# Performance work log

Measured on AMD Instinct MI355X. Metric: run time of the kernel, lower is better.

Reference implementation:

```python
import jax, jax.numpy as jnp
import numpy as np

HEADS = 8
HIDDEN = 1536
HEAD_DIM = HIDDEN // HEADS
SCALE = HEAD_DIM ** -0.5


def setup_inputs() -> dict:
    key = jax.random.key(0)
    ks = jax.random.split(key, 10)
    B, S_IMG, S_TXT = 32, 1024, 77
    w = 0.02
    return {
        "img": jax.random.normal(ks[0], (B, S_IMG, HIDDEN), dtype=jnp.float32),
        "text": jax.random.normal(ks[1], (B, S_TXT, HIDDEN), dtype=jnp.float32),
        "Wq": jax.random.normal(ks[2], (HIDDEN, HIDDEN), dtype=jnp.float32) * w,
        "bq": jnp.zeros((HIDDEN,), dtype=jnp.float32),
        "Wk": jax.random.normal(ks[3], (HIDDEN, HIDDEN), dtype=jnp.float32) * w,
        "bk": jnp.zeros((HIDDEN,), dtype=jnp.float32),
        "Wv": jax.random.normal(ks[4], (HIDDEN, HIDDEN), dtype=jnp.float32) * w,
        "bv": jnp.zeros((HIDDEN,), dtype=jnp.float32),
        "Wo": jax.random.normal(ks[5], (HIDDEN, HIDDEN), dtype=jnp.float32) * w,
        "bo": jnp.zeros((HIDDEN,), dtype=jnp.float32),
    }


def reference(img, text, Wq, bq, Wk, bk, Wv, bv, Wo, bo):
    B, Sq, D = img.shape
    Sk = text.shape[1]
    # QKV projections (nn.Linear: y = x @ W.T + b)
    q = img @ Wq.T + bq    # [B, Sq, D]
    k = text @ Wk.T + bk   # [B, Sk, D]
    v = text @ Wv.T + bv
    # detach trick: position 0 of k/v has gradient stopped; forward value unchanged
    k0 = jax.lax.stop_gradient(k[:, :1, :])
    k = jnp.concatenate([k0, k[:, 1:, :]], axis=1)
    v0 = jax.lax.stop_gradient(v[:, :1, :])
    v = jnp.concatenate([v0, v[:, 1:, :]], axis=1)
    # split heads
    q = q.reshape(B, Sq, HEADS, HEAD_DIM)
    k = k.reshape(B, Sk, HEADS, HEAD_DIM)
    v = v.reshape(B, Sk, HEADS, HEAD_DIM)
    # attention scores and probs (mask is None in this module)
    scores = jnp.einsum("bqhd,bkhd->bhqk", q, k) * SCALE  # [B, H, Sq, Sk]
    probs = jax.nn.softmax(scores, axis=-1)
    out = jnp.einsum("bhqk,bkhd->bqhd", probs, v).reshape(B, Sq, D)
    return out @ Wo.T + bo
```

## Files before the change

### kernel.cpp

```cpp
#include <hip/hip_runtime.h>
#include <hip/hip_bf16.h>


typedef unsigned short u16;
typedef _Float16 f16x8 __attribute__((ext_vector_type(8)));
typedef __attribute__((ext_vector_type(8))) short s16x8;
typedef __attribute__((ext_vector_type(4))) float f32x4;
typedef __attribute__((ext_vector_type(4))) short s16x4;

#define MFMAH(a, b, c) __builtin_amdgcn_mfma_f32_16x16x32_f16(a, b, c, 0, 0, 0)

__device__ __forceinline__ u16 f2h(float x) {
    _Float16 h = (_Float16)x;
    return __builtin_bit_cast(u16, h);
}

__device__ __forceinline__ void gload16(const u16* g, const u16* l) {
    __builtin_amdgcn_global_load_lds(
        (const __attribute__((address_space(1))) unsigned int*)g,
        (__attribute__((address_space(3))) unsigned int*)l, 16, 0, 0);
}

__device__ __forceinline__ unsigned ldsa(const u16* p) {
    return (unsigned)(size_t)(const __attribute__((address_space(3))) u16*)p;
}

__device__ __forceinline__ f16x8 dsr128(unsigned byte_addr) {
    f16x8 d;
    asm volatile("ds_read_b128 %0, %1" : "=v"(d) : "v"(byte_addr));
    return d;
}

__device__ __forceinline__ int rh(int r) { return (r >> 1) & 3; }

__global__ void conv_h(const float* __restrict__ x, u16* __restrict__ h, int n8) {
    const int i = blockIdx.x * 256 + threadIdx.x;
    if (i >= n8) return;
    const f32x4 a = ((const f32x4*)x)[2 * i];
    const f32x4 b = ((const f32x4*)x)[2 * i + 1];
    u16 o[8];
#pragma unroll
    for (int j = 0; j < 4; ++j) { o[j] = f2h(a[j]); o[4 + j] = f2h(b[j]); }
    *(s16x8*)&h[(size_t)i << 3] = *(s16x8*)o;
}

struct Conv5Args {
    const float* x[5];
    u16* h[5];
    int n8[5];
};

__global__ void conv_h5(Conv5Args A) {
    const int z = blockIdx.y;
    const int i = blockIdx.x * 256 + threadIdx.x;
    if (i >= A.n8[z]) return;
    const float* x = A.x[z];
    const f32x4 a = ((const f32x4*)x)[2 * i];
    const f32x4 b = ((const f32x4*)x)[2 * i + 1];
    u16 o[8];
#pragma unroll
    for (int j = 0; j < 4; ++j) { o[j] = f2h(a[j]); o[4 + j] = f2h(b[j]); }
    *(s16x8*)&A.h[z][(size_t)i << 3] = *(s16x8*)o;
}

template <int OUTF32>
__global__ __launch_bounds__(512, 2) void gemm_h_nt(
    const u16* __restrict__ A,
    const u16* __restrict__ B0, const float* __restrict__ bias0, void* __restrict__ C0,
    const u16* __restrict__ B1, const float* __restrict__ bias1, void* __restrict__ C1,
    int M, int N, int K, int nby) {
    __shared__ u16 lds[65536];

    const u16* B = B0; const float* bias = bias0; void* Cout = C0;
    if (blockIdx.z) { B = B1; bias = bias1; Cout = C1; }

    const int nwg = gridDim.x;
    const int q8 = nwg >> 3, r8 = nwg & 7;
    const int xcd = blockIdx.x & 7, loc = blockIdx.x >> 3;
    const int wgid = (xcd < r8 ? xcd * (q8 + 1) : r8 * (q8 + 1) + (xcd - r8) * q8) + loc;
    const int bx = wgid / nby, by = wgid - bx * nby;
    const int row0 = bx * 256, col0 = by * 256;

    const int t = threadIdx.x, lane = t & 63, w = t >> 6;
    const int wr = w >> 2, wc = w & 3;
    const int l15 = lane & 15, lhi = lane >> 4;

    const u16* gpA[2]; const u16* gpB[2];
    int lofA[2], lofB[2];
#pragma unroll
    for (int it = 0; it < 2; ++it) {
        const int ci = it * 512 + t;
        const int row = ci >> 2, slot = ci & 3;
        const int gs = slot ^ rh(row);
        int ar = row0 + row; if (ar > M - 1) ar = M - 1;
        gpA[it] = A + (size_t)ar * K + (gs << 3);
        gpB[it] = B + (size_t)(col0 + row) * K + (gs << 3);
        lofA[it] = ci * 8;
        lofB[it] = 8192 + ci * 8;
    }

    const int ss = rh(l15);
    const unsigned lb0 = ldsa(lds);
    unsigned aof[8], bof[4];
#pragma unroll
    for (int i = 0; i < 8; ++i) {
        const int ar = wr * 128 + i * 16 + l15;
        aof[i] = (unsigned)((ar * 32 + ((lhi ^ ss) << 3)) * 2);
    }
#pragma unroll
    for (int n = 0; n < 4; ++n) {
        const int br = wc * 64 + n * 16 + l15;
        bof[n] = (unsigned)((8192 + br * 32 + ((lhi ^ ss) << 3)) * 2);
    }

    f32x4 acc[8][4] = {};
    const int NT = K >> 5;

#define SBAR0() __builtin_amdgcn_sched_barrier(0)
#define BARX()  do { SBAR0(); __builtin_amdgcn_s_barrier(); SBAR0(); } while (0)
#define LGKM0() do { asm volatile("s_waitcnt lgkmcnt(0)" ::: "memory"); SBAR0(); } while (0)

#pragma unroll
    for (int p = 0; p < 3; ++p) {
        const size_t kp = (size_t)p << 5;
        u16* lb = lds + (p << 14);
        gload16(gpA[0] + kp, lb + lofA[0]); gload16(gpA[1] + kp, lb + lofA[1]);
        gload16(gpB[0] + kp, lb + lofB[0]); gload16(gpB[1] + kp, lb + lofB[1]);
    }
    asm volatile("s_waitcnt vmcnt(8)" ::: "memory");
    BARX();

    for (int tt = 0; tt < NT; ++tt) {
        const unsigned cb = lb0 + ((unsigned)(tt & 3) << 15);
        u16* lsb = lds + (((tt + 3) & 3) << 14);
        const int tx = (tt + 3 < NT) ? tt + 3 : tt + 3 - NT;
        const size_t kn = (size_t)tx << 5;

        f16x8 a0[4], a1[4], bb[4];

#pragma unroll
        for (int nf = 0; nf < 4; ++nf) bb[nf] = dsr128(cb + bof[nf]);
#pragma unroll
        for (int mf = 0; mf < 4; ++mf) a0[mf] = dsr128(cb + aof[mf]);
        SBAR0();
        gload16(gpA[0] + kn, lsb + lofA[0]);
        gload16(gpA[1] + kn, lsb + lofA[1]);
        BARX();
        LGKM0();
        __builtin_amdgcn_s_setprio(1);
#pragma unroll
        for (int nf = 0; nf < 4; ++nf)
#pragma unroll
            for (int mf = 0; mf < 4; ++mf)
                acc[mf][nf] = MFMAH(a0[mf], bb[nf], acc[mf][nf]);
        __builtin_amdgcn_s_setprio(0);
        BARX();

#pragma unroll
        for (int mf = 0; mf < 4; ++mf) a1[mf] = dsr128(cb + aof[4 + mf]);
        SBAR0();
        gload16(gpB[0] + kn, lsb + lofB[0]);
        gload16(gpB[1] + kn, lsb + lofB[1]);
        BARX();
        LGKM0();
        __builtin_amdgcn_s_setprio(1);
#pragma unroll
        for (int nf = 0; nf < 4; ++nf)
#pragma unroll
            for (int mf = 0; mf < 4; ++mf)
                acc[4 + mf][nf] = MFMAH(a1[mf], bb[nf], acc[4 + mf][nf]);
        __builtin_amdgcn_s_setprio(0);
        asm volatile("s_waitcnt vmcnt(8)" ::: "memory");
        BARX();
    }
    asm volatile("s_waitcnt vmcnt(0)" ::: "memory");

#pragma unroll
    for (int nf = 0; nf < 4; ++nf) {
        const int col = col0 + wc * 64 + nf * 16 + l15;
        const float bs = bias[col];
#pragma unroll
        for (int mf = 0; mf < 8; ++mf) {
            const int row = row0 + wr * 128 + mf * 16 + (lhi << 2);
#pragma unroll
            for (int r = 0; r < 4; ++r) {
                if (row + r < M) {
                    const float v = acc[mf][nf][r] + bs;
                    if (OUTF32) ((float*)Cout)[(size_t)(row + r) * N + col] = v;
                    else        ((u16*)Cout)[(size_t)(row + r) * N + col] = f2h(v);
                }
            }
        }
    }
#undef SBAR0
#undef BARX
#undef LGKM0
}

#define ALDK 200
#define ALDP 104

__global__ void attn_fused(const u16* __restrict__ qbuf, const u16* __restrict__ kbuf,
                           const u16* __restrict__ vbuf, u16* __restrict__ obuf) {
    __shared__ u16 Ks[80 * ALDK];
    __shared__ u16 Pls[64 * ALDP];
    __shared__ u16 Vt[96 * ALDP];

    const int t = threadIdx.x, lane = t & 63, w = t >> 6;
    const int qt = blockIdx.x, h = blockIdx.y, b = blockIdx.z;
    const int l15 = lane & 15, lhi = lane >> 4;

    f16x8 qf[6];
    {
        const size_t qrow = (size_t)(b * 1024 + qt * 64 + w * 16 + l15);
        const u16* qp = qbuf + qrow * 1536 + h * 192 + (lhi << 3);
#pragma unroll
        for (int kt = 0; kt < 6; ++kt) qf[kt] = *(const f16x8*)(qp + kt * 32);
    }

    for (int c = t; c < 80 * 24; c += 256) {
        const int s = c / 24, d8 = (c - s * 24) << 3;
        s16x8 val = {};
        if (s < 77) val = *(const s16x8*)&kbuf[(size_t)(b * 77 + s) * 1536 + h * 192 + d8];
        *(s16x8*)&Ks[s * ALDK + d8] = val;
    }
    for (int c = t; c < 96 * 12; c += 256) {
        const int s = c % 96, d8 = (c / 96) << 3;
        s16x8 val = {};
        if (s < 77) val = *(const s16x8*)&vbuf[(size_t)(b * 77 + s) * 1536 + h * 192 + d8];
#pragma unroll
        for (int j = 0; j < 8; ++j) Vt[(d8 + j) * ALDP + s] = (u16)val[j];
    }
    {
        const int row = w * 16 + l15;
        s16x4 z = {0, 0, 0, 0};
        *(s16x4*)&Pls[row * ALDP + 80 + (lhi << 2)] = z;
    }
    __syncthreads();

    f32x4 sacc[5] = {};
#pragma unroll
    for (int kt = 0; kt < 6; ++kt) {
#pragma unroll
        for (int nf = 0; nf < 5; ++nf) {
            f16x8 kf = *(const f16x8*)&Ks[(nf * 16 + l15) * ALDK + kt * 32 + (lhi << 3)];
            sacc[nf] = MFMAH(qf[kt], kf, sacc[nf]);
        }
    }

    float rps[4];
    const float scale = 0.07216878364870323f;
#pragma unroll
    for (int r = 0; r < 4; ++r) {
        float m = -1e30f;
#pragma unroll
        for (int nf = 0; nf < 5; ++nf) {
            const int c = nf * 16 + l15;
            const float sv = sacc[nf][r] * scale;
            if (c < 77) m = fmaxf(m, sv);
        }
#pragma unroll
        for (int off = 1; off < 16; off <<= 1) m = fmaxf(m, __shfl_xor(m, off));
        float sum = 0.f;
#pragma unroll
        for (int nf = 0; nf < 5; ++nf) {
            const int c = nf * 16 + l15;
            const float p = (c < 77) ? __expf(sacc[nf][r] * scale - m) : 0.f;
            sacc[nf][r] = p;
            sum += p;
        }
#pragma unroll
        for (int off = 1; off < 16; off <<= 1) sum += __shfl_xor(sum, off);
        rps[r] = 1.0f / sum;
    }

#pragma unroll
    for (int r = 0; r < 4; ++r)
#pragma unroll
        for (int nf = 0; nf < 5; ++nf)
            Pls[(w * 16 + (lhi << 2) + r) * ALDP + nf * 16 + l15] = f2h(sacc[nf][r]);
    __syncthreads();

    f16x8 pa[3];
#pragma unroll
    for (int kt = 0; kt < 3; ++kt)
        pa[kt] = *(const f16x8*)&Pls[(w * 16 + l15) * ALDP + kt * 32 + (lhi << 3)];

    const size_t orow = (size_t)(b * 1024 + qt * 64 + w * 16 + (lhi << 2));

    {
        f32x4 oacc[6] = {};
#pragma unroll
        for (int kt = 0; kt < 3; ++kt)
#pragma unroll
            for (int nf = 0; nf < 6; ++nf) {
                f16x8 vf = *(const f16x8*)&Vt[(nf * 16 + l15) * ALDP + kt * 32 + (lhi << 3)];
                oacc[nf] = MFMAH(pa[kt], vf, oacc[nf]);
            }
#pragma unroll
        for (int nf = 0; nf < 6; ++nf) {
            const int col = h * 192 + nf * 16 + l15;
#pragma unroll
            for (int r = 0; r < 4; ++r)
                obuf[(orow + r) * 1536 + col] = f2h(oacc[nf][r] * rps[r]);
        }
    }
    __syncthreads();
    for (int c = t; c < 96 * 12; c += 256) {
        const int s = c % 96, d8 = (c / 96) << 3;
        s16x8 val = {};
        if (s < 77) val = *(const s16x8*)&vbuf[(size_t)(b * 77 + s) * 1536 + h * 192 + 96 + d8];
#pragma unroll
        for (int j = 0; j < 8; ++j) Vt[(d8 + j) * ALDP + s] = (u16)val[j];
    }
    __syncthreads();
    {
        f32x4 oacc[6] = {};
#pragma unroll
        for (int kt = 0; kt < 3; ++kt)
#pragma unroll
            for (int nf = 0; nf < 6; ++nf) {
                f16x8 vf = *(const f16x8*)&Vt[(nf * 16 + l15) * ALDP + kt * 32 + (lhi << 3)];
                oacc[nf] = MFMAH(pa[kt], vf, oacc[nf]);
            }
#pragma unroll
        for (int nf = 0; nf < 6; ++nf) {
            const int col = h * 192 + 96 + nf * 16 + l15;
#pragma unroll
            for (int r = 0; r < 4; ++r)
                obuf[(orow + r) * 1536 + col] = f2h(oacc[nf][r] * rps[r]);
        }
    }
}

extern "C" void kernel_launch(void* const* d_in, const int* in_sizes, int n_in,
                              void* d_out, int out_size, void* d_ws, size_t ws_size,
                              hipStream_t stream) {
    const float* img  = (const float*)d_in[0];
    const float* text = (const float*)d_in[1];
    const float* Wq   = (const float*)d_in[2];
    const float* bq   = (const float*)d_in[3];
    const float* Wk   = (const float*)d_in[4];
    const float* bk   = (const float*)d_in[5];
    const float* Wv   = (const float*)d_in[6];
    const float* bv   = (const float*)d_in[7];
    const float* Wo   = (const float*)d_in[8];
    const float* bo   = (const float*)d_in[9];

    const size_t imgN = (size_t)32768 * 1536;
    const size_t txtN = (size_t)2464 * 1536;
    const size_t wN   = (size_t)1536 * 1536;

    u16* img_h = (u16*)d_ws;
    u16* qb    = img_h + imgN;
    u16* txt_h = qb + imgN;
    u16* Wq_h  = txt_h + txtN;
    u16* Wk_h  = Wq_h + wN;
    u16* Wv_h  = Wk_h + wN;
    u16* Wo_h  = Wv_h + wN;
    u16* kb    = Wo_h + wN;
    u16* vb    = kb + txtN;

    hipLaunchKernelGGL(conv_h, dim3((unsigned)(imgN / 8 / 256)), dim3(256),
                       0, stream, img, img_h, (int)(imgN / 8));
    Conv5Args ca;
    ca.x[0] = text; ca.h[0] = txt_h; ca.n8[0] = (int)(txtN / 8);
    ca.x[1] = Wq;   ca.h[1] = Wq_h;  ca.n8[1] = (int)(wN / 8);
    ca.x[2] = Wk;   ca.h[2] = Wk_h;  ca.n8[2] = (int)(wN / 8);
    ca.x[3] = Wv;   ca.h[3] = Wv_h;  ca.n8[3] = (int)(wN / 8);
    ca.x[4] = Wo;   ca.h[4] = Wo_h;  ca.n8[4] = (int)(wN / 8);
    hipLaunchKernelGGL(conv_h5, dim3((unsigned)((txtN / 8 + 255) / 256), 5),
                       dim3(256), 0, stream, ca);

    hipLaunchKernelGGL((gemm_h_nt<0>), dim3(768), dim3(512), 0, stream,
                       img_h, Wq_h, bq, (void*)qb, Wq_h, bq, (void*)qb,
                       32768, 1536, 1536, 6);
    hipLaunchKernelGGL((gemm_h_nt<0>), dim3(60, 1, 2), dim3(512), 0, stream,
                       txt_h, Wk_h, bk, (void*)kb, Wv_h, bv, (void*)vb,
                       2464, 1536, 1536, 6);
    hipLaunchKernelGGL(attn_fused, dim3(16, 8, 32), dim3(256), 0, stream,
                       qb, kb, vb, qb);
    hipLaunchKernelGGL((gemm_h_nt<1>), dim3(768), dim3(512), 0, stream,
                       qb, Wo_h, bo, d_out, Wo_h, bo, d_out,
                       32768, 1536, 1536, 6);
}
```

Before: 616.4 us.

## Software-pipeline LDS fragment reads across GEMM k-steps, removing intra-iteration barriers

Restructures the GEMM main loop so that the A/B fragment reads for the next k-tile are issued from LDS while the current MFMA batches run. Partial lgkmcnt waits replace the full waits, and the loop now has one barrier per iteration instead of three. The global-load wait is tightened from vmcnt(8) to vmcnt(4) to match the new placement. This is meant to hide LDS latency and cut barrier stalls, but it adds register pressure and depends on the 4-deep LDS ring staying free of read/write races.

```diff
diff --git a/kernel.cpp b/kernel.cpp
--- a/kernel.cpp
+++ b/kernel.cpp
@@ -118,7 +118,6 @@
 
 #define SBAR0() __builtin_amdgcn_sched_barrier(0)
 #define BARX()  do { SBAR0(); __builtin_amdgcn_s_barrier(); SBAR0(); } while (0)
-#define LGKM0() do { asm volatile("s_waitcnt lgkmcnt(0)" ::: "memory"); SBAR0(); } while (0)
 
 #pragma unroll
     for (int p = 0; p < 3; ++p) {
@@ -127,53 +126,58 @@
         gload16(gpA[0] + kp, lb + lofA[0]); gload16(gpA[1] + kp, lb + lofA[1]);
         gload16(gpB[0] + kp, lb + lofB[0]); gload16(gpB[1] + kp, lb + lofB[1]);
     }
-    asm volatile("s_waitcnt vmcnt(8)" ::: "memory");
+    asm volatile("s_waitcnt vmcnt(4)" ::: "memory");
     BARX();
+
+    f16x8 al[4], ah[4], bb[4];
+#pragma unroll
+    for (int nf = 0; nf < 4; ++nf) bb[nf] = dsr128(lb0 + bof[nf]);
+#pragma unroll
+    for (int mf = 0; mf < 4; ++mf) al[mf] = dsr128(lb0 + aof[mf]);
+    SBAR0();
 
     for (int tt = 0; tt < NT; ++tt) {
         const unsigned cb = lb0 + ((unsigned)(tt & 3) << 15);
+        const unsigned nb = lb0 + ((unsigned)((tt + 1) & 3) << 15);
         u16* lsb = lds + (((tt + 3) & 3) << 14);
         const int tx = (tt + 3 < NT) ? tt + 3 : tt + 3 - NT;
         const size_t kn = (size_t)tx << 5;
 
-        f16x8 a0[4], a1[4], bb[4];
-
-#pragma unroll
-        for (int nf = 0; nf < 4; ++nf) bb[nf] = dsr128(cb + bof[nf]);
-#pragma unroll
-        for (int mf = 0; mf < 4; ++mf) a0[mf] = dsr128(cb + aof[mf]);
-        SBAR0();
         gload16(gpA[0] + kn, lsb + lofA[0]);
         gload16(gpA[1] + kn, lsb + lofA[1]);
-        BARX();
-        LGKM0();
+#pragma unroll
+        for (int mf = 0; mf < 4; ++mf) ah[mf] = dsr128(cb + aof[4 + mf]);
+        SBAR0();
+        asm volatile("s_waitcnt lgkmcnt(4)" ::: "memory");
+        SBAR0();
         __builtin_amdgcn_s_setprio(1);
 #pragma unroll
         for (int nf = 0; nf < 4; ++nf)
 #pragma unroll
             for (int mf = 0; mf < 4; ++mf)
-                acc[mf][nf] = MFMAH(a0[mf], bb[nf], acc[mf][nf]);
+                acc[mf][nf] = MFMAH(al[mf], bb[nf], acc[mf][nf]);
         __builtin_amdgcn_s_setprio(0);
-        BARX();
-
-#pragma unroll
-        for (int mf = 0; mf < 4; ++mf) a1[mf] = dsr128(cb + aof[4 + mf]);
+#pragma unroll
+        for (int mf = 0; mf < 4; ++mf) al[mf] = dsr128(nb + aof[mf]);
         SBAR0();
         gload16(gpB[0] + kn, lsb + lofB[0]);
         gload16(gpB[1] + kn, lsb + lofB[1]);
+        asm volatile("s_waitcnt lgkmcnt(4)" ::: "memory");
+        SBAR0();
+        __builtin_amdgcn_s_setprio(1);
+#pragma unroll
+        for (int nf = 0; nf < 4; ++nf)
+#pragma unroll
+            for (int mf = 0; mf < 4; ++mf)
+                acc[4 + mf][nf] = MFMAH(ah[mf], bb[nf], acc[4 + mf][nf]);
+        __builtin_amdgcn_s_setprio(0);
+#pragma unroll
+        for (int nf = 0; nf < 4; ++nf) bb[nf] = dsr128(nb + bof[nf]);
+        SBAR0();
+        asm volatile("s_waitcnt vmcnt(4)" ::: "memory");
         BARX();
-        LGKM0();
-        __builtin_amdgcn_s_setprio(1);
-#pragma unroll
-        for (int nf = 0; nf < 4; ++nf)
-#pragma unroll
-            for (int mf = 0; mf < 4; ++mf)
-                acc[4 + mf][nf] = MFMAH(a1[mf], bb[nf], acc[4 + mf][nf]);
-        __builtin_amdgcn_s_setprio(0);
-        asm volatile("s_waitcnt vmcnt(8)" ::: "memory");
-        BARX();
-    }
-    asm volatile("s_waitcnt vmcnt(0)" ::: "memory");
+    }
+    asm volatile("s_waitcnt vmcnt(0) lgkmcnt(0)" ::: "memory");
 
 #pragma unroll
     for (int nf = 0; nf < 4; ++nf) {
@@ -194,7 +198,6 @@
     }
 #undef SBAR0
 #undef BARX
-#undef LGKM0
 }
 
 #define ALDK 200
```

New measurement: 606.4 us. Within noise of the previous version (-1.6%).
